# Kernel optimization log

Hardware: AMD Instinct MI355X
Metric: run time of the kernel (lower is better)

The kernel has to match this reference:

```python
import jax, jax.numpy as jnp
import numpy as np

H = 16  # n_heads


def setup_inputs() -> dict:
    key = jax.random.key(0)
    ks = jax.random.split(key, 12)
    B, S, D = 16, 512, 1024
    inp = {
        "query": jax.random.normal(ks[0], (B, S, D), jnp.float32),
        "key": jax.random.normal(ks[1], (B, S, D), jnp.float32),
        "value": jax.random.normal(ks[2], (B, S, D), jnp.float32),
        "mask": jnp.ones((B, S), dtype=bool),
        "adj": jax.random.uniform(ks[3], (B, S, S), jnp.float32),
        # nn.Linear weights are [out, in]; y = x @ W.T + b
        "Wq": jax.random.normal(ks[4], (D, D), jnp.float32) / np.sqrt(D),
        "bq": jnp.zeros((D,), jnp.float32),
        "Wk": jax.random.normal(ks[5], (D, D), jnp.float32) / np.sqrt(D),
        "bk": jnp.zeros((D,), jnp.float32),
        "Wv": jax.random.normal(ks[6], (D, D), jnp.float32) / np.sqrt(D),
        "bv": jnp.zeros((D,), jnp.float32),
        "Wo": jax.random.normal(ks[7], (D, D), jnp.float32) / np.sqrt(D),
        "bo": jnp.zeros((D,), jnp.float32),
        "beta": jnp.array([0.5], jnp.float32),  # learned residual scale (init 0 in torch)
    }
    return inp


def reference(query, key, value, mask, adj, Wq, bq, Wk, bk, Wv, bv, Wo, bo, beta):
    B, S, D = query.shape
    h = H
    dk = D // h
    N = S * dk  # channel-attention "sequence" length

    def proj(x, W, b):
        # [B,S,D] -> [B,h,S,dk]
        return (x @ W.T + b).reshape(B, S, h, dk).transpose(0, 2, 1, 3)

    Q = proj(query, Wq, bq)
    K = proj(key, Wk, bk)
    V = proj(value, Wv, bv)

    # Flatten each head: [B, h, S*dk]; torch's q,k,v are the [B,N,h] transposes.
    Qf = Q.reshape(B, h, N)
    Kf = K.reshape(B, h, N)
    Vf = V.reshape(B, h, N)

    # channel attention: scores = q^T k / sqrt(h) -> [B,h,h]
    scores = jnp.einsum("bin,bjn->bij", Qf, Kf) / jnp.sqrt(jnp.asarray(h, Qf.dtype))
    attn = jax.nn.softmax(scores, axis=-1)  # dropout is identity at eval

    # x2 = attn @ v^T -> [B,h,N] -> view [B,h,S,dk]
    x2 = jnp.einsum("bij,bjn->bin", attn, Vf).reshape(B, h, S, dk)

    x = V + beta * x2                      # scaled residual on value
    x = x.transpose(0, 2, 1, 3).reshape(B, S, D)
    out = x @ Wo.T + bo
    return out, attn
```

## Files before the change

kernel.cpp:

```cpp
#include <hip/hip_runtime.h>
#include <cstdint>
#include <cstddef>


#define DIM 1024

typedef _Float16 f16_t;
typedef _Float16 f16x4_t __attribute__((ext_vector_type(4)));
typedef _Float16 f16x8_t __attribute__((ext_vector_type(8)));
typedef float    f32x4_t __attribute__((ext_vector_type(4)));

__device__ __forceinline__ void async_ld16(const void* g, void* l) {
    __builtin_amdgcn_global_load_lds((const __attribute__((address_space(1))) void*)g,
                                     (__attribute__((address_space(3))) void*)l,
                                     16, 0, 0);
}

__global__ __launch_bounds__(256) void pack_kernel(
    const float* __restrict__ q, const float* __restrict__ k, const float* __restrict__ v,
    const float* __restrict__ Wq, const float* __restrict__ Wk,
    const float* __restrict__ Wv, const float* __restrict__ Wo,
    f16_t* __restrict__ Aq, f16_t* __restrict__ Ak, f16_t* __restrict__ Av,
    f16_t* __restrict__ Bq, f16_t* __restrict__ Bk,
    f16_t* __restrict__ Bv, f16_t* __restrict__ Bo)
{
    const int u = blockIdx.x * 256 + threadIdx.x;
    const float* src; f16_t* dst; int i;
    if (u < 2097152)      { src = q;  dst = Aq; i = u; }
    else if (u < 4194304) { src = k;  dst = Ak; i = u - 2097152; }
    else if (u < 6291456) { src = v;  dst = Av; i = u - 4194304; }
    else if (u < 6553600) { src = Wq; dst = Bq; i = u - 6291456; }
    else if (u < 6815744) { src = Wk; dst = Bk; i = u - 6553600; }
    else if (u < 7077888) { src = Wv; dst = Bv; i = u - 6815744; }
    else                  { src = Wo; dst = Bo; i = u - 7077888; }
    float4 s = ((const float4*)src)[i];
    f16x4_t h;
    h[0] = (f16_t)s.x; h[1] = (f16_t)s.y; h[2] = (f16_t)s.z; h[3] = (f16_t)s.w;
    ((f16x4_t*)dst)[i] = h;
}

__global__ __launch_bounds__(256) void gemm_f16(
    const f16_t* __restrict__ A, const f16_t* __restrict__ B,
    const float* __restrict__ bias, float* __restrict__ C)
{
    __shared__ __align__(16) f16_t As[128 * 64];
    __shared__ __align__(16) f16_t Bs[128 * 64];

    const int tid  = threadIdx.x;
    const int lane = tid & 63;
    const int w    = tid >> 6;
    const int tileM = blockIdx.x * 128;
    const int tileN = blockIdx.y * 128;
    const int wm = (w & 1) << 6;
    const int wn = (w >> 1) << 6;

    f32x4_t acc[4][4];
#pragma unroll
    for (int i = 0; i < 4; ++i)
#pragma unroll
        for (int j = 0; j < 4; ++j)
            acc[i][j] = (f32x4_t){0.f, 0.f, 0.f, 0.f};

    const int srow = lane >> 3;
    const int scol = ((lane & 7) ^ (lane >> 3)) << 3;
    const int arow = lane & 15;
    const int sx   = lane & 7;
    const int kqu  = lane >> 4;

    for (int kt = 0; kt < 16; ++kt) {
        const int k0 = kt << 6;
#pragma unroll
        for (int t = 0; t < 4; ++t) {
            const int row = (w << 5) + (t << 3);
            async_ld16(A + (size_t)(tileM + row + srow) * DIM + k0 + scol,
                       (void*)(As + row * 64));
            async_ld16(B + (size_t)(tileN + row + srow) * DIM + k0 + scol,
                       (void*)(Bs + row * 64));
        }
        __syncthreads();
#pragma unroll
        for (int kk = 0; kk < 2; ++kk) {
            const int cu = ((kk << 2) + kqu) ^ sx;
            f16x8_t af[4], bfv[4];
#pragma unroll
            for (int mt = 0; mt < 4; ++mt)
                af[mt] = *(const f16x8_t*)(As + (wm + (mt << 4) + arow) * 64 + (cu << 3));
#pragma unroll
            for (int nt = 0; nt < 4; ++nt)
                bfv[nt] = *(const f16x8_t*)(Bs + (wn + (nt << 4) + arow) * 64 + (cu << 3));
#pragma unroll
            for (int mt = 0; mt < 4; ++mt)
#pragma unroll
                for (int nt = 0; nt < 4; ++nt)
                    acc[mt][nt] = __builtin_amdgcn_mfma_f32_16x16x32_f16(
                        af[mt], bfv[nt], acc[mt][nt], 0, 0, 0);
        }
        __syncthreads();
    }

    const int rq = (lane >> 4) << 2;
#pragma unroll
    for (int nt = 0; nt < 4; ++nt) {
        const int col = tileN + wn + (nt << 4) + arow;
        const float bv = bias[col];
#pragma unroll
        for (int mt = 0; mt < 4; ++mt) {
            const int row = tileM + wm + (mt << 4) + rq;
#pragma unroll
            for (int r = 0; r < 4; ++r)
                C[(size_t)(row + r) * DIM + col] = acc[mt][nt][r] + bv;
        }
    }
}

__global__ __launch_bounds__(256) void scores_kernel(
    const float* __restrict__ Pq, const float* __restrict__ Pk,
    float* __restrict__ scores)
{
    const int b = blockIdx.x;
    const int chunk = blockIdx.y;
    const int lane = threadIdx.x & 63;
    const int w = threadIdx.x >> 6;

    float acc[16][4];
#pragma unroll
    for (int i = 0; i < 16; ++i)
#pragma unroll
        for (int jj = 0; jj < 4; ++jj) acc[i][jj] = 0.f;

    const int r0 = b * 512 + chunk * 16;
    for (int rr = 0; rr < 16; ++rr) {
        const float* qrow = Pq + (size_t)(r0 + rr) * DIM;
        const float* krow = Pk + (size_t)(r0 + rr) * DIM;
        float kv[4];
#pragma unroll
        for (int jj = 0; jj < 4; ++jj)
            kv[jj] = krow[(w * 4 + jj) * 64 + lane];
#pragma unroll
        for (int i = 0; i < 16; ++i) {
            float qv = qrow[i * 64 + lane];
#pragma unroll
            for (int jj = 0; jj < 4; ++jj) acc[i][jj] += qv * kv[jj];
        }
    }
#pragma unroll
    for (int i = 0; i < 16; ++i)
#pragma unroll
        for (int jj = 0; jj < 4; ++jj) {
            float v2 = acc[i][jj];
            for (int off = 32; off; off >>= 1) v2 += __shfl_down(v2, off);
            if (lane == 0)
                atomicAdd(&scores[b * 256 + i * 16 + w * 4 + jj], v2);
        }
}

__global__ __launch_bounds__(256) void softmax_kernel(
    const float* __restrict__ scores, const float* __restrict__ beta_p,
    float* __restrict__ attn_out, float* __restrict__ Mm)
{
    const int t = threadIdx.x;
    const int i = t & 15;
    const float beta = beta_p[0];
    float s[16];
    float mx = -1e30f;
#pragma unroll
    for (int j = 0; j < 16; ++j) {
        s[j] = scores[t * 16 + j] * 0.25f;
        mx = fmaxf(mx, s[j]);
    }
    float sum = 0.f;
#pragma unroll
    for (int j = 0; j < 16; ++j) { s[j] = expf(s[j] - mx); sum += s[j]; }
    const float inv = 1.f / sum;
#pragma unroll
    for (int j = 0; j < 16; ++j) {
        float a = s[j] * inv;
        attn_out[t * 16 + j] = a;
        Mm[t * 16 + j] = beta * a + ((j == i) ? 1.f : 0.f);
    }
}

__global__ __launch_bounds__(256) void mix_kernel(
    const float* __restrict__ Pv, const float* __restrict__ Mm,
    f16_t* __restrict__ xmix)
{
    __shared__ float Msh[256];
    const int rbase = blockIdx.x * 16;
    const int b = rbase >> 9;
    Msh[threadIdx.x] = Mm[b * 256 + threadIdx.x];
    __syncthreads();
    const int w = threadIdx.x >> 6;
    const int lane = threadIdx.x & 63;
    for (int rr = 0; rr < 4; ++rr) {
        const int r = rbase + w * 4 + rr;
        const float* vrow = Pv + (size_t)r * DIM;
        float v[16];
#pragma unroll
        for (int j = 0; j < 16; ++j) v[j] = vrow[j * 64 + lane];
#pragma unroll
        for (int i = 0; i < 16; ++i) {
            float x = 0.f;
#pragma unroll
            for (int j = 0; j < 16; ++j) x += Msh[i * 16 + j] * v[j];
            xmix[(size_t)r * DIM + i * 64 + lane] = (f16_t)x;
        }
    }
}

extern "C" void kernel_launch(void* const* d_in, const int* in_sizes, int n_in,
                              void* d_out, int out_size, void* d_ws, size_t ws_size,
                              hipStream_t stream)
{
    (void)in_sizes; (void)n_in; (void)out_size; (void)ws_size;
    const float* q    = (const float*)d_in[0];
    const float* k    = (const float*)d_in[1];
    const float* v    = (const float*)d_in[2];
    const float* Wq   = (const float*)d_in[5];
    const float* bq   = (const float*)d_in[6];
    const float* Wk   = (const float*)d_in[7];
    const float* bk   = (const float*)d_in[8];
    const float* Wv   = (const float*)d_in[9];
    const float* bv   = (const float*)d_in[10];
    const float* Wo   = (const float*)d_in[11];
    const float* bo   = (const float*)d_in[12];
    const float* beta = (const float*)d_in[13];

    float* out  = (float*)d_out;
    float* attn = (float*)d_out + 8388608;

    char* p = (char*)d_ws;
    auto take = [&](size_t n) -> char* {
        char* cur = p; p += (n + 255) & ~(size_t)255; return cur;
    };
    f16_t* Aq = (f16_t*)take(16777216);
    f16_t* Ak = (f16_t*)take(16777216);
    f16_t* Av = (f16_t*)take(16777216);
    f16_t* Bq = (f16_t*)take(2097152);
    f16_t* Bk = (f16_t*)take(2097152);
    f16_t* Bv = (f16_t*)take(2097152);
    f16_t* Bo = (f16_t*)take(2097152);
    float* Pq = (float*)take(33554432);
    float* Pk = (float*)take(33554432);
    float* Pv = (float*)take(33554432);
    float* scores = (float*)take(16384);
    float* Mm     = (float*)take(16384);
    f16_t* xmix = Aq;

    pack_kernel<<<28672, 256, 0, stream>>>(q, k, v, Wq, Wk, Wv, Wo,
                                           Aq, Ak, Av, Bq, Bk, Bv, Bo);
    hipMemsetAsync(scores, 0, 16384, stream);

    dim3 ggrid(64, 8);
    gemm_f16<<<ggrid, 256, 0, stream>>>(Aq, Bq, bq, Pq);
    gemm_f16<<<ggrid, 256, 0, stream>>>(Ak, Bk, bk, Pk);
    gemm_f16<<<ggrid, 256, 0, stream>>>(Av, Bv, bv, Pv);

    scores_kernel<<<dim3(16, 32), 256, 0, stream>>>(Pq, Pk, scores);
    softmax_kernel<<<1, 256, 0, stream>>>(scores, beta, attn, Mm);
    mix_kernel<<<512, 256, 0, stream>>>(Pv, Mm, xmix);
    gemm_f16<<<ggrid, 256, 0, stream>>>(xmix, Bo, bo, out);
}
```

Before: 338.8 us.

## Batch QKV GEMMs into one launch, fold memset into pack, widen scores/mix grids

Merges the three projection GEMMs into a single launch with a z-dimension selecting Q/K/V, so 1536 blocks run concurrently instead of three 512-block launches. It folds the scores zeroing into the pack kernel by adding 16 extra blocks, which removes the separate memset. It also halves the rows per block in the scores and mix kernels so each launches twice as many blocks. This buys more parallelism and fewer launches, at the cost of more atomic contention on scores.

```diff
diff --git a/kernel.cpp b/kernel.cpp
--- a/kernel.cpp
+++ b/kernel.cpp
@@ -22,9 +22,14 @@
     const float* __restrict__ Wv, const float* __restrict__ Wo,
     f16_t* __restrict__ Aq, f16_t* __restrict__ Ak, f16_t* __restrict__ Av,
     f16_t* __restrict__ Bq, f16_t* __restrict__ Bk,
-    f16_t* __restrict__ Bv, f16_t* __restrict__ Bo)
+    f16_t* __restrict__ Bv, f16_t* __restrict__ Bo,
+    float* __restrict__ scores)
 {
     const int u = blockIdx.x * 256 + threadIdx.x;
+    if (u >= 7340032) {
+        scores[u - 7340032] = 0.f;
+        return;
+    }
     const float* src; f16_t* dst; int i;
     if (u < 2097152)      { src = q;  dst = Aq; i = u; }
     else if (u < 4194304) { src = k;  dst = Ak; i = u - 2097152; }
@@ -39,18 +44,14 @@
     ((f16x4_t*)dst)[i] = h;
 }
 
-__global__ __launch_bounds__(256) void gemm_f16(
+__device__ __forceinline__ void gemm_body(
     const f16_t* __restrict__ A, const f16_t* __restrict__ B,
-    const float* __restrict__ bias, float* __restrict__ C)
-{
-    __shared__ __align__(16) f16_t As[128 * 64];
-    __shared__ __align__(16) f16_t Bs[128 * 64];
-
+    const float* __restrict__ bias, float* __restrict__ C,
+    f16_t* As, f16_t* Bs, int tileM, int tileN)
+{
     const int tid  = threadIdx.x;
     const int lane = tid & 63;
     const int w    = tid >> 6;
-    const int tileM = blockIdx.x * 128;
-    const int tileN = blockIdx.y * 128;
     const int wm = (w & 1) << 6;
     const int wn = (w >> 1) << 6;
 
@@ -113,6 +114,31 @@
     }
 }
 
+struct Gemm3Args {
+    const f16_t* A[3];
+    const f16_t* B[3];
+    const float* bias[3];
+    float*       C[3];
+};
+
+__global__ __launch_bounds__(256) void gemm3(Gemm3Args args)
+{
+    __shared__ __align__(16) f16_t As[128 * 64];
+    __shared__ __align__(16) f16_t Bs[128 * 64];
+    const int z = blockIdx.z;
+    gemm_body(args.A[z], args.B[z], args.bias[z], args.C[z],
+              As, Bs, blockIdx.x * 128, blockIdx.y * 128);
+}
+
+__global__ __launch_bounds__(256) void gemm_f16(
+    const f16_t* __restrict__ A, const f16_t* __restrict__ B,
+    const float* __restrict__ bias, float* __restrict__ C)
+{
+    __shared__ __align__(16) f16_t As[128 * 64];
+    __shared__ __align__(16) f16_t Bs[128 * 64];
+    gemm_body(A, B, bias, C, As, Bs, blockIdx.x * 128, blockIdx.y * 128);
+}
+
 __global__ __launch_bounds__(256) void scores_kernel(
     const float* __restrict__ Pq, const float* __restrict__ Pk,
     float* __restrict__ scores)
@@ -128,8 +154,9 @@
 #pragma unroll
         for (int jj = 0; jj < 4; ++jj) acc[i][jj] = 0.f;
 
-    const int r0 = b * 512 + chunk * 16;
-    for (int rr = 0; rr < 16; ++rr) {
+    const int r0 = b * 512 + chunk * 8;
+#pragma unroll 4
+    for (int rr = 0; rr < 8; ++rr) {
         const float* qrow = Pq + (size_t)(r0 + rr) * DIM;
         const float* krow = Pk + (size_t)(r0 + rr) * DIM;
         float kv[4];
@@ -185,14 +212,15 @@
     f16_t* __restrict__ xmix)
 {
     __shared__ float Msh[256];
-    const int rbase = blockIdx.x * 16;
+    const int rbase = blockIdx.x * 8;
     const int b = rbase >> 9;
     Msh[threadIdx.x] = Mm[b * 256 + threadIdx.x];
     __syncthreads();
     const int w = threadIdx.x >> 6;
     const int lane = threadIdx.x & 63;
-    for (int rr = 0; rr < 4; ++rr) {
-        const int r = rbase + w * 4 + rr;
+#pragma unroll
+    for (int rr = 0; rr < 2; ++rr) {
+        const int r = rbase + w * 2 + rr;
         const float* vrow = Pv + (size_t)r * DIM;
         float v[16];
 #pragma unroll
@@ -246,17 +274,18 @@
     float* Mm     = (float*)take(16384);
     f16_t* xmix = Aq;
 
-    pack_kernel<<<28672, 256, 0, stream>>>(q, k, v, Wq, Wk, Wv, Wo,
-                                           Aq, Ak, Av, Bq, Bk, Bv, Bo);
-    hipMemsetAsync(scores, 0, 16384, stream);
-
-    dim3 ggrid(64, 8);
-    gemm_f16<<<ggrid, 256, 0, stream>>>(Aq, Bq, bq, Pq);
-    gemm_f16<<<ggrid, 256, 0, stream>>>(Ak, Bk, bk, Pk);
-    gemm_f16<<<ggrid, 256, 0, stream>>>(Av, Bv, bv, Pv);
-
-    scores_kernel<<<dim3(16, 32), 256, 0, stream>>>(Pq, Pk, scores);
+    pack_kernel<<<28688, 256, 0, stream>>>(q, k, v, Wq, Wk, Wv, Wo,
+                                           Aq, Ak, Av, Bq, Bk, Bv, Bo, scores);
+
+    Gemm3Args ga;
+    ga.A[0] = Aq; ga.A[1] = Ak; ga.A[2] = Av;
+    ga.B[0] = Bq; ga.B[1] = Bk; ga.B[2] = Bv;
+    ga.bias[0] = bq; ga.bias[1] = bk; ga.bias[2] = bv;
+    ga.C[0] = Pq; ga.C[1] = Pk; ga.C[2] = Pv;
+    gemm3<<<dim3(64, 8, 3), 256, 0, stream>>>(ga);
+
+    scores_kernel<<<dim3(16, 64), 256, 0, stream>>>(Pq, Pk, scores);
     softmax_kernel<<<1, 256, 0, stream>>>(scores, beta, attn, Mm);
-    mix_kernel<<<512, 256, 0, stream>>>(Pv, Mm, xmix);
-    gemm_f16<<<ggrid, 256, 0, stream>>>(xmix, Bo, bo, out);
-}
+    mix_kernel<<<1024, 256, 0, stream>>>(Pv, Mm, xmix);
+    gemm_f16<<<dim3(64, 8), 256, 0, stream>>>(xmix, Bo, bo, out);
+}
```

After: 362.6 us. +7.0%, slower.
